# Kernel optimization log

Measured on AMD Instinct MI355X. Metric: run time of the kernel, lower is better.

## Reference

```python
import jax, jax.numpy as jnp
import numpy as np

B, S, D = 16, 4096, 512
DH = D // 2
INIT_VAR = 0.01


def setup_inputs() -> dict:
    key = jax.random.key(0)
    ks = jax.random.split(key, 6)
    x = jax.random.normal(ks[0], (B, S, D), dtype=jnp.float32)
    returns = jax.random.normal(ks[1], (B, S, D), dtype=jnp.float32)
    # GARCH params (p=q=1), initialized as in the torch module
    alpha = jnp.ones((1,), dtype=jnp.float32) * 0.1
    beta = jnp.ones((1,), dtype=jnp.float32) * 0.8
    omega = jnp.ones((1,), dtype=jnp.float32) * 0.01
    # MLP enhancement params (torch Linear default-ish init)
    lim1 = 1.0 / np.sqrt(D)
    lim2 = 1.0 / np.sqrt(DH)
    W1 = jax.random.uniform(ks[2], (D, DH), jnp.float32, -lim1, lim1)
    b1 = jax.random.uniform(ks[3], (DH,), jnp.float32, -lim1, lim1)
    W2 = jax.random.uniform(ks[4], (DH, D), jnp.float32, -lim2, lim2)
    b2 = jax.random.uniform(ks[5], (D,), jnp.float32, -lim2, lim2)
    return {"x": x, "returns": returns, "alpha": alpha, "beta": beta,
            "omega": omega, "W1": W1, "b1": b1, "W2": W2, "b2": b2}


def _cond_var(returns, alpha, beta, omega):
    # GARCH(1,1): cv[0] = INIT_VAR; cv[t] = omega + alpha*ret[t-1]^2 + beta*cv[t-1]
    ret2 = (returns[:, :-1, :] ** 2).transpose(1, 0, 2)  # [S-1, B, D] time-major
    cv0 = jnp.full(returns.shape[::2], INIT_VAR, returns.dtype)  # [B, D]

    def step(cv_prev, r2):
        cv = omega[0] + alpha[0] * r2 + beta[0] * cv_prev
        return cv, cv

    _, cvs = jax.lax.scan(step, cv0, ret2)  # [S-1, B, D]
    cond_var = jnp.concatenate([cv0[None], cvs], axis=0)  # [S, B, D]
    return cond_var.transpose(1, 0, 2)  # [B, S, D]


def reference(x, returns, alpha, beta, omega, W1, b1, W2, b2):
    cond_var = _cond_var(returns, alpha, beta, omega)
    h = jax.nn.relu(jnp.einsum('bsd,df->bsf', x, W1) + b1)
    enh = jax.nn.softplus(jnp.einsum('bsf,fd->bsd', h, W2) + b2)
    return enh * cond_var
```

## Files before the change

kernel.cpp:

```cpp
#include <hip/hip_runtime.h>
#include <hip/hip_bf16.h>
#include <hip/hip_fp16.h>

#define B_   16
#define S_   4096
#define D_   512
#define DH_  256
#define M_   (B_ * S_)
#define LC   64
#define NCH  (S_ / LC)

typedef _Float16 f16x8 __attribute__((ext_vector_type(8)));
typedef _Float16 f16x4 __attribute__((ext_vector_type(4)));
typedef float    f32x4 __attribute__((ext_vector_type(4)));

__device__ __forceinline__ void async_copy16(void* lds, const void* g) {
  __builtin_amdgcn_global_load_lds(
      (const __attribute__((address_space(1))) void*)g,
      (__attribute__((address_space(3))) void*)lds, 16, 0, 0);
}

__device__ __forceinline__ float softplus_f(float x) {
  const float t = exp2f(-fabsf(x) * 1.44269504f);
  return fmaxf(x, 0.f) + 0.69314718f * __log2f(1.f + t);
}

__global__ void transpose_to_f16(const float* __restrict__ src, _Float16* __restrict__ dst,
                                 int Rr, int Cc) {
  const int idx = blockIdx.x * 256 + threadIdx.x;
  const int c = idx / Rr;
  const int r = idx - c * Rr;
  dst[idx] = (_Float16)src[(size_t)r * Cc + c];
}

__global__ void garch_chunk(const float* __restrict__ ret,
                            const float* __restrict__ pal, const float* __restrict__ pbe,
                            const float* __restrict__ pom, float* __restrict__ Cws) {
  const int d  = threadIdx.x;
  const int bc = blockIdx.x;
  const int b  = bc >> 6;
  const int c  = bc & (NCH - 1);
  const float al = pal[0], be = pbe[0], om = pom[0];
  const float* rp = ret + ((size_t)(b * S_ + c * LC)) * D_ + d;
  float Ca = 0.f;
#pragma unroll 8
  for (int j = 0; j < LC; j++) {
    const float r = rp[(size_t)j * D_];
    Ca = fmaf(be, Ca, fmaf(al, r * r, om));
  }
  Cws[(size_t)bc * D_ + d] = Ca;
}

__global__ void garch_scan(const float* __restrict__ pbe, const float* __restrict__ Cws,
                           float* __restrict__ Vws) {
  const int d = threadIdx.x;
  const int b = blockIdx.x;
  float A = pbe[0];
  A = A * A; A = A * A; A = A * A; A = A * A; A = A * A; A = A * A;
  float V = 0.01f;
  for (int c = 0; c < NCH; c++) {
    const size_t idx = ((size_t)(b * NCH + c)) * D_ + d;
    Vws[idx] = V;
    V = fmaf(A, V, Cws[idx]);
  }
}

__global__ void garch_replay(const float* __restrict__ ret,
                             const float* __restrict__ pal, const float* __restrict__ pbe,
                             const float* __restrict__ pom, const float* __restrict__ Vws,
                             float* __restrict__ out) {
  const int d  = threadIdx.x;
  const int bc = blockIdx.x;
  const int b  = bc >> 6;
  const int c  = bc & (NCH - 1);
  const float al = pal[0], be = pbe[0], om = pom[0];
  const size_t base = ((size_t)(b * S_ + c * LC)) * D_ + d;
  float v = Vws[(size_t)bc * D_ + d];
  out[base] = v;
  const float* rp = ret + base;
#pragma unroll 8
  for (int j = 1; j < LC; j++) {
    const float r = rp[(size_t)(j - 1) * D_];
    v = fmaf(be, v, fmaf(al, r * r, om));
    out[base + (size_t)j * D_] = v;
  }
}

template<int KDIM, int NOUT, int MODE>
__launch_bounds__(256, 3)
__global__ void gemm_f16(const void* __restrict__ Ap, const _Float16* __restrict__ Bt,
                         const float* __restrict__ bias, const float* cvin,
                         void* outp) {
  __shared__ __align__(16) char smem[32768];
  _Float16* As = (_Float16*)smem;
  _Float16* Bs = (_Float16*)(smem + 16384);
  float*    Cs = (float*)smem;

  const int tid  = threadIdx.x;
  const int lane = tid & 63;
  const int w    = tid >> 6;
  const int wm   = w >> 1, wn = w & 1;
  const size_t m0 = (size_t)blockIdx.x * 128;
  const int    n0 = blockIdx.y * 128;

  f32x4 acc[4][4];
#pragma unroll
  for (int i = 0; i < 4; i++)
#pragma unroll
    for (int j = 0; j < 4; j++)
      acc[i][j] = (f32x4){0.f, 0.f, 0.f, 0.f};

  const _Float16* hA = (const _Float16*)Ap;
  const float*    fA = (const float*)Ap;

  for (int kt = 0; kt < KDIM; kt += 64) {
#pragma unroll
    for (int rr = 0; rr < 4; rr++) {
      const int task = rr * 256 + tid;
      const int row = task >> 3, pos = task & 7;
      const int dc = pos ^ (row & 7);
      async_copy16(&Bs[task * 8], &Bt[(size_t)(n0 + row) * KDIM + kt + dc * 8]);
    }
    if (MODE == 1) {
#pragma unroll
      for (int rr = 0; rr < 4; rr++) {
        const int task = rr * 256 + tid;
        const int row = task >> 3, pos = task & 7;
        const int dc = pos ^ (row & 7);
        async_copy16(&As[task * 8], &hA[(m0 + row) * (size_t)KDIM + kt + dc * 8]);
      }
    } else {
#pragma unroll
      for (int rr = 0; rr < 4; rr++) {
        const int task = rr * 256 + tid;
        const int row = task >> 3, dc = task & 7;
        const float* sp = &fA[(m0 + row) * (size_t)KDIM + kt + dc * 8];
        const float4 v0 = *(const float4*)(sp);
        const float4 v1 = *(const float4*)(sp + 4);
        f16x8 hv;
        hv[0] = (_Float16)v0.x; hv[1] = (_Float16)v0.y;
        hv[2] = (_Float16)v0.z; hv[3] = (_Float16)v0.w;
        hv[4] = (_Float16)v1.x; hv[5] = (_Float16)v1.y;
        hv[6] = (_Float16)v1.z; hv[7] = (_Float16)v1.w;
        const int pos = dc ^ (row & 7);
        *(f16x8*)&As[row * 64 + pos * 8] = hv;
      }
    }
    __syncthreads();

    f16x8 af[4][2], bf[4][2];
#pragma unroll
    for (int f = 0; f < 4; f++) {
#pragma unroll
      for (int kk = 0; kk < 2; kk++) {
        const int k8 = kk * 4 + (lane >> 4);
        const int ar = wm * 64 + f * 16 + (lane & 15);
        af[f][kk] = *(const f16x8*)&As[ar * 64 + ((k8 ^ (ar & 7)) * 8)];
        const int br = wn * 64 + f * 16 + (lane & 15);
        bf[f][kk] = *(const f16x8*)&Bs[br * 64 + ((k8 ^ (br & 7)) * 8)];
      }
    }
#pragma unroll
    for (int kk = 0; kk < 2; kk++)
#pragma unroll
      for (int fm = 0; fm < 4; fm++)
#pragma unroll
        for (int fn = 0; fn < 4; fn++)
          acc[fm][fn] = __builtin_amdgcn_mfma_f32_16x16x32_f16(af[fm][kk], bf[fn][kk],
                                                               acc[fm][fn], 0, 0, 0);
    __syncthreads();
  }

  for (int p = 0; p < 2; ++p) {
    if (p) __syncthreads();
    if (wn == p) {
#pragma unroll
      for (int fm = 0; fm < 4; fm++) {
#pragma unroll
        for (int fn = 0; fn < 4; fn++) {
          const int colL = fn * 16 + (lane & 15);
          const float bv = bias[n0 + p * 64 + colL];
          const int c2 = colL ^ ((lane >> 4) << 4);
#pragma unroll
          for (int j = 0; j < 4; j++) {
            const int row = wm * 64 + fm * 16 + (lane >> 4) * 4 + j;
            Cs[row * 64 + c2] = acc[fm][fn][j] + bv;
          }
        }
      }
    }
    __syncthreads();
#pragma unroll
    for (int k = 0; k < 8; k++) {
      const int f   = k * 256 + tid;
      const int row = f >> 4;
      const int c0  = (f & 15) * 4;
      const int c2  = c0 ^ (((row >> 2) & 3) << 4);
      const f32x4 v = *(const f32x4*)&Cs[row * 64 + c2];
      const size_t gbase = (m0 + row) * (size_t)NOUT + n0 + p * 64 + c0;
      if (MODE == 0) {
        f16x4 hv;
        hv[0] = (_Float16)fmaxf(v[0], 0.f);
        hv[1] = (_Float16)fmaxf(v[1], 0.f);
        hv[2] = (_Float16)fmaxf(v[2], 0.f);
        hv[3] = (_Float16)fmaxf(v[3], 0.f);
        *(f16x4*)&((_Float16*)outp)[gbase] = hv;
      } else {
        const f32x4 cv4 = *(const f32x4*)&cvin[gbase];
        f32x4 o;
        o[0] = softplus_f(v[0]) * cv4[0];
        o[1] = softplus_f(v[1]) * cv4[1];
        o[2] = softplus_f(v[2]) * cv4[2];
        o[3] = softplus_f(v[3]) * cv4[3];
        *(f32x4*)&((float*)outp)[gbase] = o;
      }
    }
  }
}

extern "C" void kernel_launch(void* const* d_in, const int* in_sizes, int n_in,
                              void* d_out, int out_size, void* d_ws, size_t ws_size,
                              hipStream_t stream) {
  const float* x     = (const float*)d_in[0];
  const float* rets  = (const float*)d_in[1];
  const float* alpha = (const float*)d_in[2];
  const float* beta  = (const float*)d_in[3];
  const float* omega = (const float*)d_in[4];
  const float* W1    = (const float*)d_in[5];
  const float* b1    = (const float*)d_in[6];
  const float* W2    = (const float*)d_in[7];
  const float* b2    = (const float*)d_in[8];
  float* out = (float*)d_out;

  char* ws = (char*)d_ws;
  _Float16* W1T = (_Float16*)ws;
  _Float16* W2T = (_Float16*)(ws + (256 << 10));
  float*    Cws = (float*)(ws + (512 << 10));
  float*    Vws = (float*)(ws + (512 << 10) + (2 << 20));
  _Float16* h   = (_Float16*)(ws + (512 << 10) + (4 << 20));

  transpose_to_f16<<<512, 256, 0, stream>>>(W1, W1T, 512, 256);
  transpose_to_f16<<<512, 256, 0, stream>>>(W2, W2T, 256, 512);

  garch_chunk <<<B_ * NCH, 512, 0, stream>>>(rets, alpha, beta, omega, Cws);
  garch_scan  <<<B_,       512, 0, stream>>>(beta, Cws, Vws);
  garch_replay<<<B_ * NCH, 512, 0, stream>>>(rets, alpha, beta, omega, Vws, out);

  gemm_f16<512, 256, 0><<<dim3(M_ / 128, 2), 256, 0, stream>>>(x, W1T, b1, nullptr, h);
  gemm_f16<256, 512, 1><<<dim3(M_ / 128, 4), 256, 0, stream>>>(h, W2T, b2, out, out);
}
```

Baseline: 466.8 us.

## Fuse GARCH replay into second GEMM epilogue, drop separate replay kernel

Removes the garch_replay kernel, which wrote the full conditional variance tensor to the output buffer that the second GEMM then read back. The second GEMM's epilogue now stages the full 128x128 tile in 64KB LDS and has each thread walk one column across 64 rows, recomputing the GARCH recurrence from the chunk start value while applying softplus. This avoids a full write plus read of the cond_var tensor. In exchange, the epilogue reads returns serially, LDS grows to 64KB, and occupancy for this kernel drops to 2 blocks per CU.

Result: faster. 421.7 us (-9.6%).

```diff
diff --git a/kernel.cpp b/kernel.cpp
--- a/kernel.cpp
+++ b/kernel.cpp
@@ -65,36 +65,18 @@
   }
 }
 
-__global__ void garch_replay(const float* __restrict__ ret,
-                             const float* __restrict__ pal, const float* __restrict__ pbe,
-                             const float* __restrict__ pom, const float* __restrict__ Vws,
-                             float* __restrict__ out) {
-  const int d  = threadIdx.x;
-  const int bc = blockIdx.x;
-  const int b  = bc >> 6;
-  const int c  = bc & (NCH - 1);
-  const float al = pal[0], be = pbe[0], om = pom[0];
-  const size_t base = ((size_t)(b * S_ + c * LC)) * D_ + d;
-  float v = Vws[(size_t)bc * D_ + d];
-  out[base] = v;
-  const float* rp = ret + base;
-#pragma unroll 8
-  for (int j = 1; j < LC; j++) {
-    const float r = rp[(size_t)(j - 1) * D_];
-    v = fmaf(be, v, fmaf(al, r * r, om));
-    out[base + (size_t)j * D_] = v;
-  }
-}
-
 template<int KDIM, int NOUT, int MODE>
-__launch_bounds__(256, 3)
+__launch_bounds__(256, MODE ? 2 : 3)
 __global__ void gemm_f16(const void* __restrict__ Ap, const _Float16* __restrict__ Bt,
-                         const float* __restrict__ bias, const float* cvin,
+                         const float* __restrict__ bias,
+                         const float* __restrict__ retp,
+                         const float* __restrict__ Vws_g,
+                         const float* __restrict__ gal, const float* __restrict__ gbe,
+                         const float* __restrict__ gom,
                          void* outp) {
-  __shared__ __align__(16) char smem[32768];
+  __shared__ __align__(16) char smem[MODE ? 65536 : 32768];
   _Float16* As = (_Float16*)smem;
   _Float16* Bs = (_Float16*)(smem + 16384);
-  float*    Cs = (float*)smem;
 
   const int tid  = threadIdx.x;
   const int lane = tid & 63;
@@ -171,48 +153,75 @@
     __syncthreads();
   }
 
-  for (int p = 0; p < 2; ++p) {
-    if (p) __syncthreads();
-    if (wn == p) {
-#pragma unroll
-      for (int fm = 0; fm < 4; fm++) {
-#pragma unroll
-        for (int fn = 0; fn < 4; fn++) {
-          const int colL = fn * 16 + (lane & 15);
-          const float bv = bias[n0 + p * 64 + colL];
-          const int c2 = colL ^ ((lane >> 4) << 4);
-#pragma unroll
-          for (int j = 0; j < 4; j++) {
-            const int row = wm * 64 + fm * 16 + (lane >> 4) * 4 + j;
-            Cs[row * 64 + c2] = acc[fm][fn][j] + bv;
+  if (MODE == 1) {
+    float* Cs = (float*)smem;
+#pragma unroll
+    for (int fm = 0; fm < 4; fm++)
+#pragma unroll
+      for (int fn = 0; fn < 4; fn++) {
+        const int colG = wn * 64 + fn * 16 + (lane & 15);
+        const float bv = bias[n0 + colG];
+#pragma unroll
+        for (int j = 0; j < 4; j++) {
+          const int rloc = fm * 16 + (lane >> 4) * 4 + j;
+          const int colS = colG ^ (((rloc >> 2) & 3) << 4);
+          Cs[wm * 8192 + rloc * 128 + colS] = acc[fm][fn][j] + bv;
+        }
+      }
+    __syncthreads();
+    const int half = tid >> 7;
+    const int col  = tid & 127;
+    const int d    = n0 + col;
+    const size_t mrow0 = m0 + half * 64;
+    const int b  = (int)(m0 >> 12);
+    const int ch = (int)((m0 & 4095) >> 6) + half;
+    float V = Vws_g[((size_t)(b * NCH + ch)) * D_ + d];
+    const float al = gal[0], be = gbe[0], om = gom[0];
+    float* oo = (float*)outp;
+#pragma unroll 8
+    for (int j = 0; j < LC; j++) {
+      const size_t gidx = (mrow0 + j) * (size_t)D_ + d;
+      const int colS = col ^ (((j >> 2) & 3) << 4);
+      const float a = Cs[half * 8192 + j * 128 + colS];
+      oo[gidx] = softplus_f(a) * V;
+      const float r = retp[gidx];
+      V = fmaf(be, V, fmaf(al * r, r, om));
+    }
+  } else {
+    float* Cs = (float*)smem;
+    for (int p = 0; p < 2; ++p) {
+      if (p) __syncthreads();
+      if (wn == p) {
+#pragma unroll
+        for (int fm = 0; fm < 4; fm++) {
+#pragma unroll
+          for (int fn = 0; fn < 4; fn++) {
+            const int colL = fn * 16 + (lane & 15);
+            const float bv = bias[n0 + p * 64 + colL];
+            const int c2 = colL ^ ((lane >> 4) << 4);
+#pragma unroll
+            for (int j = 0; j < 4; j++) {
+              const int row = wm * 64 + fm * 16 + (lane >> 4) * 4 + j;
+              Cs[row * 64 + c2] = acc[fm][fn][j] + bv;
+            }
           }
         }
       }
-    }
-    __syncthreads();
-#pragma unroll
-    for (int k = 0; k < 8; k++) {
-      const int f   = k * 256 + tid;
-      const int row = f >> 4;
-      const int c0  = (f & 15) * 4;
-      const int c2  = c0 ^ (((row >> 2) & 3) << 4);
-      const f32x4 v = *(const f32x4*)&Cs[row * 64 + c2];
-      const size_t gbase = (m0 + row) * (size_t)NOUT + n0 + p * 64 + c0;
-      if (MODE == 0) {
+      __syncthreads();
+#pragma unroll
+      for (int k = 0; k < 8; k++) {
+        const int f   = k * 256 + tid;
+        const int row = f >> 4;
+        const int c0  = (f & 15) * 4;
+        const int c2  = c0 ^ (((row >> 2) & 3) << 4);
+        const f32x4 v = *(const f32x4*)&Cs[row * 64 + c2];
+        const size_t gbase = (m0 + row) * (size_t)NOUT + n0 + p * 64 + c0;
         f16x4 hv;
         hv[0] = (_Float16)fmaxf(v[0], 0.f);
         hv[1] = (_Float16)fmaxf(v[1], 0.f);
         hv[2] = (_Float16)fmaxf(v[2], 0.f);
         hv[3] = (_Float16)fmaxf(v[3], 0.f);
         *(f16x4*)&((_Float16*)outp)[gbase] = hv;
-      } else {
-        const f32x4 cv4 = *(const f32x4*)&cvin[gbase];
-        f32x4 o;
-        o[0] = softplus_f(v[0]) * cv4[0];
-        o[1] = softplus_f(v[1]) * cv4[1];
-        o[2] = softplus_f(v[2]) * cv4[2];
-        o[3] = softplus_f(v[3]) * cv4[3];
-        *(f32x4*)&((float*)outp)[gbase] = o;
       }
     }
   }
@@ -244,8 +253,9 @@
 
   garch_chunk <<<B_ * NCH, 512, 0, stream>>>(rets, alpha, beta, omega, Cws);
   garch_scan  <<<B_,       512, 0, stream>>>(beta, Cws, Vws);
-  garch_replay<<<B_ * NCH, 512, 0, stream>>>(rets, alpha, beta, omega, Vws, out);
-
-  gemm_f16<512, 256, 0><<<dim3(M_ / 128, 2), 256, 0, stream>>>(x, W1T, b1, nullptr, h);
-  gemm_f16<256, 512, 1><<<dim3(M_ / 128, 4), 256, 0, stream>>>(h, W2T, b2, out, out);
-}
+
+  gemm_f16<512, 256, 0><<<dim3(M_ / 128, 2), 256, 0, stream>>>(
+      x, W1T, b1, nullptr, nullptr, nullptr, nullptr, nullptr, h);
+  gemm_f16<256, 512, 1><<<dim3(M_ / 128, 4), 256, 0, stream>>>(
+      h, W2T, b2, rets, Vws, alpha, beta, omega, out);
+}
```
